# Kernel tuning notes

Hardware: AMD Instinct MI355X
Metric: run time of the kernel (lower is better)

Reference implementation:

```python
import jax, jax.numpy as jnp
import numpy as np

B = 2048
IN = 1024
M = 256
P = M * (M + 1) // 2  # 32896 Cholesky params


def setup_inputs() -> dict:
    key = jax.random.key(0)
    k1, k2, k3 = jax.random.split(key, 3)
    x = jax.random.normal(k1, (B, IN), dtype=jnp.float32)
    # nn.Linear(input_size, P): weight [P, IN], bias [P]
    bound = 1.0 / np.sqrt(IN)
    W = jax.random.uniform(k2, (P, IN), dtype=jnp.float32, minval=-bound, maxval=bound)
    b = jax.random.uniform(k3, (P,), dtype=jnp.float32, minval=-bound, maxval=bound)
    return {"x": x, "W": W, "b": b}


def reference(x, W, b):
    # Linear projection to packed lower-triangular params [B, P]
    chol_params = x @ W.T + b
    # Row-major lower-triangular fill order matches the torch double loop:
    # (0,0),(1,0),(1,1),(2,0),...
    rows, cols = jnp.tril_indices(M)
    diag_mask = rows == cols  # [P]
    vals = jnp.where(diag_mask[None, :], jax.nn.relu(chol_params), chol_params)
    L = jnp.zeros((x.shape[0], M, M), dtype=chol_params.dtype)
    L = L.at[:, rows, cols].set(vals)
    # Batched L @ L^T -> positive semi-definite matrix [B, M, M]
    return jnp.einsum('bik,bjk->bij', L, L)
```

## Files before the change

kernel.cpp:

```cpp
#include <hip/hip_runtime.h>

#define B_DIM 2048
#define IN_DIM 1024
#define M_DIM 256
#define P_DIM 32896
#define RTP_B 40960
#define CRTP_BYTES (167772160)
#define WB_BYTES   (67371008)

typedef __attribute__((ext_vector_type(8))) short short8;
typedef __attribute__((ext_vector_type(4))) float f32x4;

#define GLD16(gsrc, ldst) __builtin_amdgcn_global_load_lds(                    \
    (const __attribute__((address_space(1))) unsigned int*)(gsrc),             \
    (__attribute__((address_space(3))) unsigned int*)(ldst), 16, 0, 0)

__device__ __forceinline__ unsigned short f2bf(float f) {
    unsigned int u = __float_as_uint(f);
    u += 0x7FFFu + ((u >> 16) & 1u);
    return (unsigned short)(u >> 16);
}
__device__ __forceinline__ int rtp0(int r) {
    const int g = r >> 6;
    return 2048 * g * (g + 1) + (r & 63) * ((g + 1) << 6);
}
__device__ __forceinline__ int rtp_off(int r, int c) {
    return rtp0(r) + (((c >> 3) ^ (r & 7)) << 3) + (c & 7);
}

__global__ void pad_zero(unsigned short* __restrict__ Crtp) {
    const int r = threadIdx.x;
    const int b = blockIdx.x;
    const int g = r >> 6;
    const int nch = (g + 1) << 3;
    const int xm = r & 7;
    unsigned short* base = Crtp + (size_t)b * RTP_B + rtp0(r);
    const int pc = (r >> 3) ^ xm;
    for (int c = r + 1; (c >> 3) == (r >> 3); ++c) base[(pc << 3) + (c & 7)] = 0;
    const uint4 z = make_uint4(0u, 0u, 0u, 0u);
    for (int cc = (r >> 3) + 1; cc < nch; ++cc)
        *reinterpret_cast<uint4*>(&base[(cc ^ xm) << 3]) = z;
}

__global__ void prep_x(const float* __restrict__ X, unsigned short* __restrict__ Xhi) {
    const int i = blockIdx.x * blockDim.x + threadIdx.x;
    float4 v = reinterpret_cast<const float4*>(X)[i];
    ushort4 h;
    h.x = f2bf(v.x); h.y = f2bf(v.y); h.z = f2bf(v.z); h.w = f2bf(v.w);
    reinterpret_cast<ushort4*>(Xhi)[i] = h;
}

__global__ void prep_w(const float* __restrict__ W, unsigned short* __restrict__ Wb) {
    const int i = blockIdx.x * blockDim.x + threadIdx.x;
    float4 v = reinterpret_cast<const float4*>(W)[i];
    ushort4 h;
    h.x = f2bf(v.x); h.y = f2bf(v.y); h.z = f2bf(v.z); h.w = f2bf(v.w);
    reinterpret_cast<ushort4*>(Wb)[i] = h;
}

__global__ __launch_bounds__(512) void gemm1_kernel(
    const unsigned short* __restrict__ Xhi,
    const unsigned short* __restrict__ Wb, const float* __restrict__ bias,
    unsigned short* __restrict__ Crtp)
{
    __shared__ unsigned short lds[3 * 24576];

    const int lin = blockIdx.x;
    const int x   = lin & 7;
    const int j   = lin >> 3;
    const int rtile = ((x & 1) << 2) + (j & 3);
    const int panel = (x >> 1) * 65 + (j >> 2);
    if (panel >= 257) return;
    const int row0 = rtile << 8;
    const int col0 = panel << 7;

    const int tid  = threadIdx.x;
    const int lane = tid & 63;
    const int wid  = tid >> 6;
    const int wr   = wid >> 1;
    const int wc   = wid & 1;
    const int lr16 = lane & 15;
    const int kc   = lane >> 4;

    const int srow = lane >> 3;
    const int sch  = (lane & 7) ^ srow;
    const unsigned short* gsrc[6];
    int loff[6];
#pragma unroll
    for (int i = 0; i < 6; ++i) {
        const int c = 6 * wid + i;
        if (c < 32) {
            gsrc[i] = Xhi + (size_t)(row0 + c * 8 + srow) * IN_DIM + (sch << 3);
            loff[i] = c * 512;
        } else {
            gsrc[i] = Wb + (size_t)(col0 + (c - 32) * 8 + srow) * IN_DIM + (sch << 3);
            loff[i] = 16384 + (c - 32) * 512;
        }
    }

#define STAGE(kt, bufo)                                                        \
    {                                                                          \
        _Pragma("unroll")                                                      \
        for (int i = 0; i < 6; ++i)                                            \
            GLD16(gsrc[i] + ((kt) << 6), &lds[(bufo) + loff[i]]);              \
    }

    f32x4 acc[4][4];
#pragma unroll
    for (int m = 0; m < 4; ++m)
#pragma unroll
        for (int n = 0; n < 4; ++n) acc[m][n] = (f32x4){0.f, 0.f, 0.f, 0.f};

    int o0 = 0, o1 = 24576, o2 = 49152;
    STAGE(0, o0);
    STAGE(1, o1);

    for (int it = 0; it < 16; ++it) {
        if (it < 15) asm volatile("s_waitcnt vmcnt(6)" ::: "memory");
        else         asm volatile("s_waitcnt vmcnt(0)" ::: "memory");
        __builtin_amdgcn_s_barrier();
        asm volatile("" ::: "memory");

        const int cb = o0;
        short8 av[4], bv[4];
#pragma unroll
        for (int m = 0; m < 4; ++m) {
            const int r = (wr << 6) + (m << 4) + lr16;
            av[m] = *reinterpret_cast<const short8*>(&lds[cb + r * 64 + (kc ^ (r & 7)) * 8]);
        }
#pragma unroll
        for (int n = 0; n < 4; ++n) {
            const int r = (wc << 6) + (n << 4) + lr16;
            bv[n] = *reinterpret_cast<const short8*>(&lds[cb + 16384 + r * 64 + (kc ^ (r & 7)) * 8]);
        }
        if (it < 14) STAGE(it + 2, o2);
        __builtin_amdgcn_s_setprio(1);
#pragma unroll
        for (int m = 0; m < 4; ++m)
#pragma unroll
            for (int n = 0; n < 4; ++n)
                acc[m][n] = __builtin_amdgcn_mfma_f32_16x16x32_bf16(av[m], bv[n], acc[m][n], 0, 0, 0);
        __builtin_amdgcn_s_setprio(0);

#pragma unroll
        for (int m = 0; m < 4; ++m) {
            const int r = (wr << 6) + (m << 4) + lr16;
            av[m] = *reinterpret_cast<const short8*>(&lds[cb + r * 64 + ((4 + kc) ^ (r & 7)) * 8]);
        }
#pragma unroll
        for (int n = 0; n < 4; ++n) {
            const int r = (wc << 6) + (n << 4) + lr16;
            bv[n] = *reinterpret_cast<const short8*>(&lds[cb + 16384 + r * 64 + ((4 + kc) ^ (r & 7)) * 8]);
        }
        __builtin_amdgcn_s_setprio(1);
#pragma unroll
        for (int m = 0; m < 4; ++m)
#pragma unroll
            for (int n = 0; n < 4; ++n)
                acc[m][n] = __builtin_amdgcn_mfma_f32_16x16x32_bf16(av[m], bv[n], acc[m][n], 0, 0, 0);
        __builtin_amdgcn_s_setprio(0);

        const int t = o0; o0 = o1; o1 = o2; o2 = t;
    }
#undef STAGE

#pragma unroll
    for (int n = 0; n < 4; ++n) {
        const int p = col0 + (wc << 6) + (n << 4) + lr16;
        const float t = sqrtf((float)(8 * p + 1));
        const int rt = (int)((t - 1.0f) * 0.5f + 0.001f);
        const int ct = p - ((rt * (rt + 1)) >> 1);
        const int off = rtp_off(rt, ct);
        const bool diag = (ct == rt);
        const float bvs = bias[p];
#pragma unroll
        for (int m = 0; m < 4; ++m) {
#pragma unroll
            for (int q = 0; q < 4; ++q) {
                const int brow = row0 + (wr << 6) + (m << 4) + (kc << 2) + q;
                float v = acc[m][n][q] + bvs;
                if (diag) v = fmaxf(v, 0.f);
                Crtp[(size_t)brow * RTP_B + off] = f2bf(v);
            }
        }
    }
}

__global__ __launch_bounds__(256) void syrk_kernel(
    const unsigned short* __restrict__ Crtp, float* __restrict__ O)
{
    __shared__ unsigned short Lt[RTP_B];
    const int tid  = threadIdx.x;
    const int lane = tid & 63;
    const int wid  = tid >> 6;
    const int b    = blockIdx.x;
    const unsigned short* Cb = Crtp + (size_t)b * RTP_B;

#pragma unroll
    for (int i = 0; i < 20; ++i) {
        const int g = wid * 20 + i;
        GLD16(Cb + g * 512 + (lane << 3), &Lt[g * 512]);
    }
    __syncthreads();

    const int lr16 = lane & 15;
    const int kc   = lane >> 4;
    float* Ob = O + (size_t)b * (M_DIM * M_DIM);

    const unsigned char LIST[4][5] = {
        {0x33, 0x22, 0x00, 0x00, 0x00},
        {0x23, 0x32, 0x01, 0x10, 0x00},
        {0x11, 0x12, 0x21, 0x02, 0x00},
        {0x13, 0x31, 0x03, 0x30, 0x20}};
    const int CNT[4] = {3, 4, 4, 5};
    const int cnt = CNT[wid];

    for (int tt = 0; tt < cnt; ++tt) {
        const int code = LIST[wid][tt];
        const int ti = code >> 4, tj = code & 15;

        int baseA[4], xA[4], baseB[4], xB[4];
#pragma unroll
        for (int m = 0; m < 4; ++m) {
            const int ia = (ti << 6) + (m << 4) + lr16;
            const int jb = (tj << 6) + (m << 4) + lr16;
            baseA[m] = rtp0(ia); xA[m] = ia & 7;
            baseB[m] = rtp0(jb); xB[m] = jb & 7;
        }
        f32x4 acc[4][4];
#pragma unroll
        for (int m = 0; m < 4; ++m)
#pragma unroll
            for (int n = 0; n < 4; ++n) acc[m][n] = (f32x4){0.f, 0.f, 0.f, 0.f};

        const int kmax = ti < tj ? ti : tj;
        for (int kt = 0; kt <= kmax; ++kt) {
#pragma unroll
            for (int s = 0; s < 2; ++s) {
                const int cidx = (kt << 3) + (s << 2) + kc;
                short8 a[4], bb[4];
#pragma unroll
                for (int m = 0; m < 4; ++m)
                    a[m] = *reinterpret_cast<const short8*>(&Lt[baseA[m] + ((cidx ^ xA[m]) << 3)]);
#pragma unroll
                for (int n = 0; n < 4; ++n)
                    bb[n] = *reinterpret_cast<const short8*>(&Lt[baseB[n] + ((cidx ^ xB[n]) << 3)]);
#pragma unroll
                for (int m = 0; m < 4; ++m)
#pragma unroll
                    for (int n = 0; n < 4; ++n)
                        acc[m][n] = __builtin_amdgcn_mfma_f32_16x16x32_bf16(a[m], bb[n], acc[m][n], 0, 0, 0);
            }
        }
#pragma unroll
        for (int m = 0; m < 4; ++m) {
            const int i0 = (ti << 6) + (m << 4) + (kc << 2);
#pragma unroll
            for (int n = 0; n < 4; ++n) {
                const int j = (tj << 6) + (n << 4) + lr16;
#pragma unroll
                for (int q = 0; q < 4; ++q)
                    __builtin_nontemporal_store(acc[m][n][q], &Ob[(size_t)(i0 + q) * M_DIM + j]);
            }
        }
    }
}

extern "C" void kernel_launch(void* const* d_in, const int* in_sizes, int n_in,
                              void* d_out, int out_size, void* d_ws, size_t ws_size,
                              hipStream_t stream)
{
    (void)in_sizes; (void)n_in; (void)out_size; (void)ws_size;
    const float* x    = (const float*)d_in[0];
    const float* W    = (const float*)d_in[1];
    const float* bias = (const float*)d_in[2];
    float* O = (float*)d_out;

    char* ws = (char*)d_ws;
    unsigned short* Crtp = (unsigned short*)ws;
    unsigned short* Wb   = (unsigned short*)(ws + CRTP_BYTES);
    unsigned short* Xhi  = (unsigned short*)(ws + CRTP_BYTES + WB_BYTES);

    pad_zero<<<B_DIM, 256, 0, stream>>>(Crtp);
    prep_x<<<(B_DIM * IN_DIM / 4) / 256, 256, 0, stream>>>(x, Xhi);
    prep_w<<<(P_DIM * IN_DIM / 4) / 256, 256, 0, stream>>>(W, Wb);
    gemm1_kernel<<<dim3(2080), dim3(512), 0, stream>>>(Xhi, Wb, bias, Crtp);
    syrk_kernel<<<dim3(B_DIM), dim3(256), 0, stream>>>(Crtp, O);
}
```

Measured before the change: 402.9 us.

## Enlarge GEMM tile to 256x256 with K=32 stages and fuse prep kernels

Merges the three prep kernels (W and X bf16 conversion plus Crtp padding) into one launch and adds zero-padding of W up to 33024 rows. The GEMM tile grows from 256x128 to 256x256 with a K-step of 32 per stage, so each wave holds 4x8 accumulators and W is reused across more output columns. The block-swizzled grid mapping is dropped and out-of-range columns are skipped in the epilogue. This cuts launch overhead and global reloads, at the cost of higher register pressure and twice as many barriers per K.

```diff
diff --git a/kernel.cpp b/kernel.cpp
--- a/kernel.cpp
+++ b/kernel.cpp
@@ -4,9 +4,10 @@
 #define IN_DIM 1024
 #define M_DIM 256
 #define P_DIM 32896
+#define NPAD 33024
 #define RTP_B 40960
 #define CRTP_BYTES (167772160)
-#define WB_BYTES   (67371008)
+#define WB_BYTES   (67633152)
 
 typedef __attribute__((ext_vector_type(8))) short short8;
 typedef __attribute__((ext_vector_type(4))) float f32x4;
@@ -28,34 +29,51 @@
     return rtp0(r) + (((c >> 3) ^ (r & 7)) << 3) + (c & 7);
 }
 
-__global__ void pad_zero(unsigned short* __restrict__ Crtp) {
-    const int r = threadIdx.x;
-    const int b = blockIdx.x;
-    const int g = r >> 6;
-    const int nch = (g + 1) << 3;
-    const int xm = r & 7;
-    unsigned short* base = Crtp + (size_t)b * RTP_B + rtp0(r);
-    const int pc = (r >> 3) ^ xm;
-    for (int c = r + 1; (c >> 3) == (r >> 3); ++c) base[(pc << 3) + (c & 7)] = 0;
-    const uint4 z = make_uint4(0u, 0u, 0u, 0u);
-    for (int cc = (r >> 3) + 1; cc < nch; ++cc)
-        *reinterpret_cast<uint4*>(&base[(cc ^ xm) << 3]) = z;
-}
-
-__global__ void prep_x(const float* __restrict__ X, unsigned short* __restrict__ Xhi) {
-    const int i = blockIdx.x * blockDim.x + threadIdx.x;
-    float4 v = reinterpret_cast<const float4*>(X)[i];
-    ushort4 h;
-    h.x = f2bf(v.x); h.y = f2bf(v.y); h.z = f2bf(v.z); h.w = f2bf(v.w);
-    reinterpret_cast<ushort4*>(Xhi)[i] = h;
-}
-
-__global__ void prep_w(const float* __restrict__ W, unsigned short* __restrict__ Wb) {
-    const int i = blockIdx.x * blockDim.x + threadIdx.x;
-    float4 v = reinterpret_cast<const float4*>(W)[i];
-    ushort4 h;
-    h.x = f2bf(v.x); h.y = f2bf(v.y); h.z = f2bf(v.z); h.w = f2bf(v.w);
-    reinterpret_cast<ushort4*>(Wb)[i] = h;
+#define NW_BLK 8224
+#define NX_BLK 512
+#define NP_BLK 16
+#define NZ_BLK 2048
+__global__ void prep_all(const float* __restrict__ X, const float* __restrict__ W,
+                         unsigned short* __restrict__ Xhi, unsigned short* __restrict__ Wb,
+                         unsigned short* __restrict__ Crtp) {
+    const int bid = blockIdx.x, tid = threadIdx.x;
+    if (bid < NW_BLK) {
+#pragma unroll
+        for (int u = 0; u < 4; ++u) {
+            const int i = bid * 1024 + u * 256 + tid;
+            float4 v = reinterpret_cast<const float4*>(W)[i];
+            ushort4 h;
+            h.x = f2bf(v.x); h.y = f2bf(v.y); h.z = f2bf(v.z); h.w = f2bf(v.w);
+            reinterpret_cast<ushort4*>(Wb)[i] = h;
+        }
+    } else if (bid < NW_BLK + NX_BLK) {
+#pragma unroll
+        for (int u = 0; u < 4; ++u) {
+            const int i = (bid - NW_BLK) * 1024 + u * 256 + tid;
+            float4 v = reinterpret_cast<const float4*>(X)[i];
+            ushort4 h;
+            h.x = f2bf(v.x); h.y = f2bf(v.y); h.z = f2bf(v.z); h.w = f2bf(v.w);
+            reinterpret_cast<ushort4*>(Xhi)[i] = h;
+        }
+    } else if (bid < NW_BLK + NX_BLK + NP_BLK) {
+        uint4* dst = reinterpret_cast<uint4*>(Wb + (size_t)P_DIM * IN_DIM);
+        const uint4 z = make_uint4(0u, 0u, 0u, 0u);
+#pragma unroll
+        for (int u = 0; u < 4; ++u)
+            dst[((bid - NW_BLK - NX_BLK) * 256 + tid) * 4 + u] = z;
+    } else {
+        const int b = bid - NW_BLK - NX_BLK - NP_BLK;
+        const int r = tid;
+        const int g = r >> 6;
+        const int nch = (g + 1) << 3;
+        const int xm = r & 7;
+        unsigned short* base = Crtp + (size_t)b * RTP_B + rtp0(r);
+        const int pc = (r >> 3) ^ xm;
+        for (int c = r + 1; (c >> 3) == (r >> 3); ++c) base[(pc << 3) + (c & 7)] = 0;
+        const uint4 z = make_uint4(0u, 0u, 0u, 0u);
+        for (int cc = (r >> 3) + 1; cc < nch; ++cc)
+            *reinterpret_cast<uint4*>(&base[(cc ^ xm) << 3]) = z;
+    }
 }
 
 __global__ __launch_bounds__(512) void gemm1_kernel(
@@ -63,110 +81,82 @@
     const unsigned short* __restrict__ Wb, const float* __restrict__ bias,
     unsigned short* __restrict__ Crtp)
 {
-    __shared__ unsigned short lds[3 * 24576];
+    __shared__ unsigned short lds[3 * 16384];
 
     const int lin = blockIdx.x;
-    const int x   = lin & 7;
-    const int j   = lin >> 3;
-    const int rtile = ((x & 1) << 2) + (j & 3);
-    const int panel = (x >> 1) * 65 + (j >> 2);
-    if (panel >= 257) return;
-    const int row0 = rtile << 8;
-    const int col0 = panel << 7;
+    const int row0 = (lin & 7) << 8;
+    const int col0 = (lin >> 3) << 8;
 
     const int tid  = threadIdx.x;
     const int lane = tid & 63;
     const int wid  = tid >> 6;
-    const int wr   = wid >> 1;
-    const int wc   = wid & 1;
+    const int wr   = wid & 3;
+    const int wc   = wid >> 2;
     const int lr16 = lane & 15;
     const int kc   = lane >> 4;
 
-    const int srow = lane >> 3;
-    const int sch  = (lane & 7) ^ srow;
-    const unsigned short* gsrc[6];
-    int loff[6];
-#pragma unroll
-    for (int i = 0; i < 6; ++i) {
-        const int c = 6 * wid + i;
-        if (c < 32) {
-            gsrc[i] = Xhi + (size_t)(row0 + c * 8 + srow) * IN_DIM + (sch << 3);
-            loff[i] = c * 512;
-        } else {
-            gsrc[i] = Wb + (size_t)(col0 + (c - 32) * 8 + srow) * IN_DIM + (sch << 3);
-            loff[i] = 16384 + (c - 32) * 512;
-        }
-    }
+    const int srow = lane >> 2;
+    const int sch  = (lane & 3) ^ ((lane >> 3) & 3);
+    const unsigned short* gA = Xhi + (size_t)(row0 + wid * 32 + srow) * IN_DIM + (sch << 3);
+    const unsigned short* gB = Wb  + (size_t)(col0 + wid * 32 + srow) * IN_DIM + (sch << 3);
+    const int la = (wid * 32) * 32;
+    const int lb = 8192 + (wid * 32) * 32;
 
 #define STAGE(kt, bufo)                                                        \
     {                                                                          \
-        _Pragma("unroll")                                                      \
-        for (int i = 0; i < 6; ++i)                                            \
-            GLD16(gsrc[i] + ((kt) << 6), &lds[(bufo) + loff[i]]);              \
-    }
-
-    f32x4 acc[4][4];
+        GLD16(gA + (kt) * 32,                 &lds[(bufo) + la]);              \
+        GLD16(gA + 16 * IN_DIM + (kt) * 32,   &lds[(bufo) + la + 512]);        \
+        GLD16(gB + (kt) * 32,                 &lds[(bufo) + lb]);              \
+        GLD16(gB + 16 * IN_DIM + (kt) * 32,   &lds[(bufo) + lb + 512]);        \
+    }
+
+    f32x4 acc[4][8];
 #pragma unroll
     for (int m = 0; m < 4; ++m)
 #pragma unroll
-        for (int n = 0; n < 4; ++n) acc[m][n] = (f32x4){0.f, 0.f, 0.f, 0.f};
-
-    int o0 = 0, o1 = 24576, o2 = 49152;
+        for (int n = 0; n < 8; ++n) acc[m][n] = (f32x4){0.f, 0.f, 0.f, 0.f};
+
+    int o0 = 0, o1 = 16384, o2 = 32768;
     STAGE(0, o0);
     STAGE(1, o1);
 
-    for (int it = 0; it < 16; ++it) {
-        if (it < 15) asm volatile("s_waitcnt vmcnt(6)" ::: "memory");
+    for (int it = 0; it < 32; ++it) {
+        if (it < 31) asm volatile("s_waitcnt vmcnt(4)" ::: "memory");
         else         asm volatile("s_waitcnt vmcnt(0)" ::: "memory");
         __builtin_amdgcn_s_barrier();
         asm volatile("" ::: "memory");
 
         const int cb = o0;
-        short8 av[4], bv[4];
+        short8 av[4], bv[8];
 #pragma unroll
         for (int m = 0; m < 4; ++m) {
             const int r = (wr << 6) + (m << 4) + lr16;
-            av[m] = *reinterpret_cast<const short8*>(&lds[cb + r * 64 + (kc ^ (r & 7)) * 8]);
-        }
-#pragma unroll
-        for (int n = 0; n < 4; ++n) {
-            const int r = (wc << 6) + (n << 4) + lr16;
-            bv[n] = *reinterpret_cast<const short8*>(&lds[cb + 16384 + r * 64 + (kc ^ (r & 7)) * 8]);
-        }
-        if (it < 14) STAGE(it + 2, o2);
+            av[m] = *reinterpret_cast<const short8*>(
+                &lds[cb + r * 32 + ((kc ^ ((r >> 1) & 3)) << 3)]);
+        }
+#pragma unroll
+        for (int n = 0; n < 8; ++n) {
+            const int r = (wc << 7) + (n << 4) + lr16;
+            bv[n] = *reinterpret_cast<const short8*>(
+                &lds[cb + 8192 + r * 32 + ((kc ^ ((r >> 1) & 3)) << 3)]);
+        }
+        if (it < 30) STAGE(it + 2, o2);
         __builtin_amdgcn_s_setprio(1);
 #pragma unroll
         for (int m = 0; m < 4; ++m)
 #pragma unroll
-            for (int n = 0; n < 4; ++n)
+            for (int n = 0; n < 8; ++n)
                 acc[m][n] = __builtin_amdgcn_mfma_f32_16x16x32_bf16(av[m], bv[n], acc[m][n], 0, 0, 0);
         __builtin_amdgcn_s_setprio(0);
 
-#pragma unroll
-        for (int m = 0; m < 4; ++m) {
-            const int r = (wr << 6) + (m << 4) + lr16;
-            av[m] = *reinterpret_cast<const short8*>(&lds[cb + r * 64 + ((4 + kc) ^ (r & 7)) * 8]);
-        }
-#pragma unroll
-        for (int n = 0; n < 4; ++n) {
-            const int r = (wc << 6) + (n << 4) + lr16;
-            bv[n] = *reinterpret_cast<const short8*>(&lds[cb + 16384 + r * 64 + ((4 + kc) ^ (r & 7)) * 8]);
-        }
-        __builtin_amdgcn_s_setprio(1);
-#pragma unroll
-        for (int m = 0; m < 4; ++m)
-#pragma unroll
-            for (int n = 0; n < 4; ++n)
-                acc[m][n] = __builtin_amdgcn_mfma_f32_16x16x32_bf16(av[m], bv[n], acc[m][n], 0, 0, 0);
-        __builtin_amdgcn_s_setprio(0);
-
         const int t = o0; o0 = o1; o1 = o2; o2 = t;
     }
 #undef STAGE
 
 #pragma unroll
-    for (int n = 0; n < 4; ++n) {
-        const int p = col0 + (wc << 6) + (n << 4) + lr16;
+    for (int n = 0; n < 8; ++n) {
+        const int p = col0 + (wc << 7) + (n << 4) + lr16;
+        if (p >= P_DIM) continue;
         const float t = sqrtf((float)(8 * p + 1));
         const int rt = (int)((t - 1.0f) * 0.5f + 0.001f);
         const int ct = p - ((rt * (rt + 1)) >> 1);
@@ -281,9 +271,8 @@
     unsigned short* Wb   = (unsigned short*)(ws + CRTP_BYTES);
     unsigned short* Xhi  = (unsigned short*)(ws + CRTP_BYTES + WB_BYTES);
 
-    pad_zero<<<B_DIM, 256, 0, stream>>>(Crtp);
-    prep_x<<<(B_DIM * IN_DIM / 4) / 256, 256, 0, stream>>>(x, Xhi);
-    prep_w<<<(P_DIM * IN_DIM / 4) / 256, 256, 0, stream>>>(W, Wb);
-    gemm1_kernel<<<dim3(2080), dim3(512), 0, stream>>>(Xhi, Wb, bias, Crtp);
+    prep_all<<<dim3(NW_BLK + NX_BLK + NP_BLK + NZ_BLK), dim3(256), 0, stream>>>(
+        x, W, Xhi, Wb, Crtp);
+    gemm1_kernel<<<dim3(1032), dim3(512), 0, stream>>>(Xhi, Wb, bias, Crtp);
     syrk_kernel<<<dim3(B_DIM), dim3(256), 0, stream>>>(Crtp, O);
 }
```

Result: slower. 428.6 us (+6.4%).
